# Optimization experiments

Hardware: AMD Instinct MI355X
Metric: run time of the kernel (lower is better)

The kernel has to match this reference:

```python
import jax, jax.numpy as jnp
import numpy as np

EPS = 1e-5

def _bn(h, gamma, beta):
    # training-mode batch norm over dim 0 (biased variance, as torch)
    mu = h.mean(axis=0)
    var = ((h - mu) ** 2).mean(axis=0)
    return (h - mu) * jax.lax.rsqrt(var + EPS) * gamma + beta

def _mlp(h, W1, b1, g1, be1, W2, b2):
    # PyG MLP, num_layers=2: Linear -> BatchNorm -> ReLU -> Linear (dropout=0)
    h = h @ W1 + b1
    h = jax.nn.relu(_bn(h, g1, be1))
    return h @ W2 + b2

def setup_inputs() -> dict:
    key = jax.random.key(0)
    ks = jax.random.split(key, 12)
    N, E = 50000, 800000
    node_dim, edge_dim, hidden = 64, 64, 128
    d_in1 = node_dim + edge_dim   # 128
    d_in2 = node_dim + hidden     # 192
    def lin(k, fi, fo):
        s = 1.0 / np.sqrt(fi)
        return jax.random.uniform(k, (fi, fo), jnp.float32, -s, s)
    inp = {
        "x": jax.random.normal(ks[0], (N, node_dim), jnp.float32),
        "edge_index": jax.random.randint(ks[1], (2, E), 0, N, jnp.int32),
        "edge_attr": jax.random.normal(ks[2], (E, edge_dim), jnp.float32),
        "u": jax.random.normal(ks[3], (1, 16), jnp.float32),
        "batch": jnp.zeros((N,), jnp.int32),
        # node_mlp_1 params
        "W1a": lin(ks[4], d_in1, hidden), "b1a": jnp.zeros((hidden,), jnp.float32),
        "g1a": jnp.ones((hidden,), jnp.float32), "be1a": jnp.zeros((hidden,), jnp.float32),
        "W2a": lin(ks[5], hidden, hidden), "b2a": jnp.zeros((hidden,), jnp.float32),
        # node_mlp_2 params
        "W1b": lin(ks[6], d_in2, hidden), "b1b": jnp.zeros((hidden,), jnp.float32),
        "g1b": jnp.ones((hidden,), jnp.float32), "be1b": jnp.zeros((hidden,), jnp.float32),
        "W2b": lin(ks[7], hidden, node_dim), "b2b": jnp.zeros((node_dim,), jnp.float32),
    }
    return inp

def reference(x, edge_index, edge_attr, u, batch,
              W1a, b1a, g1a, be1a, W2a, b2a,
              W1b, b1b, g1b, be1b, W2b, b2b):
    row, col = edge_index[0], edge_index[1]
    # gather source nodes, concat edge features  -> [E, node_dim+edge_dim]
    out = jnp.concatenate([x[row], edge_attr], axis=1)
    out = _mlp(out, W1a, b1a, g1a, be1a, W2a, b2a)          # [E, hidden]
    out = jax.ops.segment_sum(out, col, num_segments=x.shape[0])  # scatter_add -> [N, hidden]
    out = jnp.concatenate([x, out], axis=1)                  # [N, node_dim+hidden]
    return _mlp(out, W1b, b1b, g1b, be1b, W2b, b2b)          # [N, node_dim]
```

## Files before the change

kernel.cpp:

```cpp
#include <hip/hip_runtime.h>
#include <hip/hip_fp16.h>


typedef _Float16 half8  __attribute__((ext_vector_type(8)));
typedef _Float16 half4h __attribute__((ext_vector_type(4)));
typedef float    floatx4 __attribute__((ext_vector_type(4)));

#define MFMA16(a, b, c) __builtin_amdgcn_mfma_f32_16x16x32_f16(a, b, c, 0, 0, 0)

#define LDS_BARRIER() do { \
    asm volatile("s_waitcnt lgkmcnt(0)" ::: "memory"); \
    __builtin_amdgcn_s_barrier(); \
} while (0)

__device__ __forceinline__ float col_reduce16(float v) {
    v += __shfl_xor(v, 16, 64);
    v += __shfl_xor(v, 32, 64);
    return v;
}

__global__ void k_prep(const float* __restrict__ w1a, const float* __restrict__ w2a,
                       const float* __restrict__ w1b, const float* __restrict__ w2b,
                       _Float16* __restrict__ w1at, _Float16* __restrict__ w2at,
                       _Float16* __restrict__ w1bt, _Float16* __restrict__ w2bt) {
    int i = blockIdx.x * 256 + threadIdx.x;
    if (i < 16384) {
        int n = i >> 7, k = i & 127;
        w1at[n * 128 + k] = (_Float16)w1a[k * 128 + n];
    } else if (i < 32768) {
        int j = i - 16384; int n = j >> 7, k = j & 127;
        w2at[n * 128 + k] = (_Float16)w2a[k * 128 + n];
    } else if (i < 57344) {
        int j = i - 32768; int n = j / 192, k = j - n * 192;
        w1bt[n * 192 + k] = (_Float16)w1b[k * 128 + n];
    } else if (i < 65536) {
        int j = i - 57344; int n = j >> 7, k = j & 127;
        w2bt[n * 128 + k] = (_Float16)w2b[k * 64 + n];
    }
}

__global__ __launch_bounds__(1024) void k_scan(const int* __restrict__ cnt,
                                               int* __restrict__ cur, int N) {
    __shared__ int sp[1024];
    int t = threadIdx.x;
    int chunk = (N + 1023) >> 10;
    int base = t * chunk;
    int s = 0;
    for (int j = 0; j < chunk; j++) {
        int idx = base + j;
        if (idx < N) s += cnt[idx];
    }
    sp[t] = s; __syncthreads();
    for (int off = 1; off < 1024; off <<= 1) {
        int v = (t >= off) ? sp[t - off] : 0;
        __syncthreads();
        sp[t] += v;
        __syncthreads();
    }
    int run = sp[t] - s;
    for (int j = 0; j < chunk; j++) {
        int idx = base + j;
        if (idx < N) { cur[idx] = run; run += cnt[idx]; }
    }
}

__global__ void k_scatter_fin(const int* __restrict__ rowi, const int* __restrict__ coli,
                              int* __restrict__ cur, int2* __restrict__ pairs,
                              const float* __restrict__ sums, const float* __restrict__ sqs,
                              const float* __restrict__ gamma, const float* __restrict__ beta,
                              float* __restrict__ scale, float* __restrict__ shift,
                              float count, int E) {
    int i = blockIdx.x * 512 + threadIdx.x;
    if (i < E) {
        int c = coli[i];
        int p = atomicAdd(&cur[c], 1);
        pairs[p] = make_int2(i, (c << 16) | rowi[i]);
    }
    if (blockIdx.x == 0 && threadIdx.x < 128) {
        int j = threadIdx.x;
        float s = 0.f, ssq = 0.f;
        for (int k = 0; k < 16; k++) { s += sums[k * 128 + j]; ssq += sqs[k * 128 + j]; }
        float mu = s / count;
        float var = ssq / count - mu * mu;
        float sc = gamma[j] * rsqrtf(var + 1e-5f);
        scale[j] = sc;
        shift[j] = beta[j] - mu * sc;
    }
}

__global__ __launch_bounds__(512, 4) void k_edge_stats(
    const float* __restrict__ x, const int* __restrict__ rowi,
    const int* __restrict__ coli,
    const float* __restrict__ ea, const _Float16* __restrict__ w1t,
    float* __restrict__ gsum, float* __restrict__ gsq,
    int* __restrict__ cnt, int nTiles) {
    __shared__ _Float16 sW[128][136];
    __shared__ _Float16 sIn[128][136];
    const int tid = threadIdx.x, lane = tid & 63, wv = tid >> 6;
    const int lm = lane & 15, q = lane >> 4, koff = q * 8;
    const int G = gridDim.x;
    const int e = tid >> 2, part = tid & 3;

    {
        int n = tid >> 2, seg = (tid & 3) * 32;
        const half8* src = (const half8*)(w1t + n * 128 + seg);
        half8* dst = (half8*)&sW[n][seg];
        dst[0] = src[0]; dst[1] = src[1]; dst[2] = src[2]; dst[3] = src[3];
    }
    float sAcc[8], ssAcc[8];
#pragma unroll
    for (int i = 0; i < 8; i++) { sAcc[i] = 0.f; ssAcc[i] = 0.f; }

    int t = blockIdx.x;
    floatx4 pv[8];
    int hc = 0;
    {
        long ge = (long)t * 128 + e;
        const float* src = (part < 2) ? x + (long)rowi[ge] * 64 + part * 32
                                      : ea + ge * 64 + (part - 2) * 32;
#pragma unroll
        for (int i = 0; i < 8; i++) pv[i] = ((const floatx4*)src)[i];
        if (part == 0) hc = coli[ge];
    }
    for (; t < nTiles; t += G) {
        {
            _Float16* dst = &sIn[e][part * 32];
#pragma unroll
            for (int i = 0; i < 8; i++) {
                half4h h = {(_Float16)pv[i][0], (_Float16)pv[i][1],
                            (_Float16)pv[i][2], (_Float16)pv[i][3]};
                *(half4h*)(dst + i * 4) = h;
            }
        }
        LDS_BARRIER();
        if (part == 0) atomicAdd(&cnt[hc], 1);
        int tn = t + G;
        if (tn < nTiles) {
            long ge = (long)tn * 128 + e;
            const float* src = (part < 2) ? x + (long)rowi[ge] * 64 + part * 32
                                          : ea + ge * 64 + (part - 2) * 32;
#pragma unroll
            for (int i = 0; i < 8; i++) pv[i] = ((const floatx4*)src)[i];
            if (part == 0) hc = coli[ge];
        }
        half8 a[4];
#pragma unroll
        for (int kb = 0; kb < 4; kb++)
            a[kb] = *(const half8*)&sIn[wv * 16 + lm][kb * 32 + koff];
#pragma unroll
        for (int nt = 0; nt < 8; nt++) {
            floatx4 acc = {0.f, 0.f, 0.f, 0.f};
            const int c = nt * 16 + lm;
#pragma unroll
            for (int kb = 0; kb < 4; kb++) {
                half8 b = *(const half8*)&sW[c][kb * 32 + koff];
                acc = MFMA16(a[kb], b, acc);
            }
            sAcc[nt]  += acc[0] + acc[1] + acc[2] + acc[3];
            ssAcc[nt] += acc[0]*acc[0] + acc[1]*acc[1] + acc[2]*acc[2] + acc[3]*acc[3];
        }
        LDS_BARRIER();
    }
#pragma unroll
    for (int nt = 0; nt < 8; nt++) {
        float s  = col_reduce16(sAcc[nt]);
        float ss = col_reduce16(ssAcc[nt]);
        if (q == 0) {
            int c = nt * 16 + lm;
            int slot = (blockIdx.x * 8 + wv) & 15;
            unsafeAtomicAdd(&gsum[slot * 128 + c], s);
            unsafeAtomicAdd(&gsq[slot * 128 + c], ss);
        }
    }
}

__global__ void k_finalize(const float* __restrict__ sums, const float* __restrict__ sqs,
                           const float* __restrict__ gamma, const float* __restrict__ beta,
                           float* __restrict__ scale, float* __restrict__ shift, float count) {
    int i = threadIdx.x;
    float s = 0.f, ssq = 0.f;
    for (int j = 0; j < 16; j++) { s += sums[j * 128 + i]; ssq += sqs[j * 128 + i]; }
    float mu = s / count;
    float var = ssq / count - mu * mu;
    float sc = gamma[i] * rsqrtf(var + 1e-5f);
    scale[i] = sc;
    shift[i] = beta[i] - mu * sc;
}

__global__ __launch_bounds__(512, 2) void k_edge_mlp(
    const float* __restrict__ x, const int2* __restrict__ pairs,
    const float* __restrict__ ea, const _Float16* __restrict__ w1t, const _Float16* __restrict__ w2t,
    const float* __restrict__ scale, const float* __restrict__ shift, const float* __restrict__ b2a,
    __half* __restrict__ agg, int nTiles) {
    __shared__ _Float16 sW1[128][136];
    __shared__ _Float16 sW2[128][136];
    __shared__ _Float16 sIn[2][128][136];
    __shared__ float sScale[128], sShift[128], sB2[128];
    __shared__ int sCol[2][128];
    const int tid = threadIdx.x, lane = tid & 63, wv = tid >> 6;
    const int lm = lane & 15, q = lane >> 4, koff = q * 8;
    const int G = gridDim.x;
    const int e = tid >> 2, part = tid & 3;

    {
        int n = tid >> 2, seg = (tid & 3) * 32;
        const half8* s1 = (const half8*)(w1t + n * 128 + seg);
        half8* d1 = (half8*)&sW1[n][seg];
        d1[0] = s1[0]; d1[1] = s1[1]; d1[2] = s1[2]; d1[3] = s1[3];
        const half8* s2 = (const half8*)(w2t + n * 128 + seg);
        half8* d2 = (half8*)&sW2[n][seg];
        d2[0] = s2[0]; d2[1] = s2[1]; d2[2] = s2[2]; d2[3] = s2[3];
    }
    if (tid < 128) { sScale[tid] = scale[tid]; sShift[tid] = shift[tid]; sB2[tid] = b2a[tid]; }

    int t = blockIdx.x;
    {
        long ge = (long)t * 128 + e;
        int2 pr = pairs[ge];
        const float* src = (part < 2) ? x + (long)(pr.y & 0xFFFF) * 64 + part * 32
                                      : ea + (long)pr.x * 64 + (part - 2) * 32;
        _Float16* dst = &sIn[0][e][part * 32];
#pragma unroll
        for (int i = 0; i < 8; i++) {
            floatx4 v = ((const floatx4*)src)[i];
            half4h h = {(_Float16)v[0], (_Float16)v[1], (_Float16)v[2], (_Float16)v[3]};
            *(half4h*)(dst + i * 4) = h;
        }
        if (tid < 128) sCol[0][tid] = (int)(((unsigned)pairs[(long)t * 128 + tid].y) >> 16);
    }
    __syncthreads();
    int p = 0;
    for (; t < nTiles; t += G) {
        half8 a[4];
#pragma unroll
        for (int kb = 0; kb < 4; kb++)
            a[kb] = *(const half8*)&sIn[p][wv * 16 + lm][kb * 32 + koff];
        int myCol[4];
        const int m0 = wv * 16 + q * 4;
#pragma unroll
        for (int r = 0; r < 4; r++) myCol[r] = sCol[p][m0 + r];
        int cp = sCol[p][(q > 0) ? m0 - 1 : m0];
        int cn = sCol[p][(q < 3) ? m0 + 4 : m0 + 3];
        const bool h0 = (q == 0) || (myCol[0] != cp);
        const bool h1 = myCol[1] != myCol[0];
        const bool h2 = myCol[2] != myCol[1];
        const bool h3 = myCol[3] != myCol[2];
        const bool t0 = h1, t1 = h2, t2 = h3;
        const bool t3 = (q == 3) || (myCol[3] != cn);
        const bool c0m = !h0, c1m = c0m && !h1, c2m = c1m && !h2, c3m = c2m && !h3;
        const int F0 = (h0 | h1 | h2 | h3) ? 1 : 0;
        int Fp1 = __shfl(F0, (lane - 16) & 63, 64);
        const bool add1 = (q >= 1) && !F0;
        const int F1 = (F0 || ((q >= 1) && Fp1)) ? 1 : 0;
        const bool add2 = (q >= 2) && !F1;
        const bool useC = (q >= 1) && !h0;

        int tn = t + G; bool hasNext = tn < nTiles;
        floatx4 pv[8]; int pcol = 0;
        if (hasNext) {
            long ge = (long)tn * 128 + e;
            int2 pr = pairs[ge];
            const float* src = (part < 2) ? x + (long)(pr.y & 0xFFFF) * 64 + part * 32
                                          : ea + (long)pr.x * 64 + (part - 2) * 32;
#pragma unroll
            for (int i = 0; i < 8; i++) pv[i] = ((const floatx4*)src)[i];
            if (tid < 128) pcol = (int)(((unsigned)pairs[(long)tn * 128 + tid].y) >> 16);
        }
        floatx4 acc1[8];
#pragma unroll
        for (int nt = 0; nt < 8; nt++) {
            floatx4 acc = {0.f, 0.f, 0.f, 0.f};
            const int c = nt * 16 + lm;
#pragma unroll
            for (int kb = 0; kb < 4; kb++) {
                half8 b = *(const half8*)&sW1[c][kb * 32 + koff];
                acc = MFMA16(a[kb], b, acc);
            }
            acc1[nt] = acc;
        }
        LDS_BARRIER();

        _Float16(*sT)[136] = sIn[p];
#pragma unroll
        for (int nt = 0; nt < 8; nt++) {
            const int c = nt * 16 + lm;
            float sc = sScale[c], sh = sShift[c];
            half4h h;
#pragma unroll
            for (int r = 0; r < 4; r++)
                h[r] = (_Float16)fmaxf(acc1[nt][r] * sc + sh, 0.f);
            *(half4h*)&sT[c][wv * 16 + q * 4] = h;
        }
        half8 a2[4];
#pragma unroll
        for (int kb = 0; kb < 4; kb++) {
#pragma unroll
            for (int j = 0; j < 8; j++)
                a2[kb][j] = sT[kb * 32 + koff + j][wv * 16 + lm];
        }
#pragma unroll
        for (int nt = 0; nt < 8; nt++) {
            floatx4 acc = {0.f, 0.f, 0.f, 0.f};
            const int c = nt * 16 + lm;
#pragma unroll
            for (int kb = 0; kb < 4; kb++) {
                half8 b = *(const half8*)&sW2[c][kb * 32 + koff];
                acc = MFMA16(a2[kb], b, acc);
            }
            acc1[nt] = acc;
        }
        if (hasNext) {
            _Float16* dst = &sIn[p ^ 1][e][part * 32];
#pragma unroll
            for (int i = 0; i < 8; i++) {
                half4h h = {(_Float16)pv[i][0], (_Float16)pv[i][1],
                            (_Float16)pv[i][2], (_Float16)pv[i][3]};
                *(half4h*)(dst + i * 4) = h;
            }
            if (tid < 128) sCol[p ^ 1][tid] = pcol;
        }
#pragma unroll
        for (int nt = 0; nt < 8; nt++) {
            const int c = nt * 16 + lm;
            const int c0 = c & ~1;
            float bb = sB2[c];
            float v0 = acc1[nt][0] + bb, v1 = acc1[nt][1] + bb;
            float v2 = acc1[nt][2] + bb, v3 = acc1[nt][3] + bb;
            float s0 = v0;
            float s1 = h1 ? v1 : (s0 + v1);
            float s2 = h2 ? v2 : (s1 + v2);
            float s3 = h3 ? v3 : (s2 + v3);
            float S = s3;
            float Sp = __shfl(S, (lane - 16) & 63, 64);
            if (add1) S += Sp;
            float Sq = __shfl(S, (lane - 32) & 63, 64);
            if (add2) S += Sq;
            float Cc = __shfl(S, (lane - 16) & 63, 64);
            float C = useC ? Cc : 0.f;
            float f0 = c0m ? (s0 + C) : s0;
            float f1 = c1m ? (s1 + C) : s1;
            float f2 = c2m ? (s2 + C) : s2;
            float f3 = c3m ? (s3 + C) : s3;
            float g0 = __shfl_xor(f0, 1, 64), g1 = __shfl_xor(f1, 1, 64);
            float g2 = __shfl_xor(f2, 1, 64), g3 = __shfl_xor(f3, 1, 64);
            if ((lane & 1) == 0) {
                if (t0) unsafeAtomicAdd((__half2*)&agg[(size_t)myCol[0] * 128 + c0], __floats2half2_rn(f0, g0));
                if (t1) unsafeAtomicAdd((__half2*)&agg[(size_t)myCol[1] * 128 + c0], __floats2half2_rn(f1, g1));
            } else {
                if (t2) unsafeAtomicAdd((__half2*)&agg[(size_t)myCol[2] * 128 + c0], __floats2half2_rn(g2, f2));
                if (t3) unsafeAtomicAdd((__half2*)&agg[(size_t)myCol[3] * 128 + c0], __floats2half2_rn(g3, f3));
            }
        }
        LDS_BARRIER();
        p ^= 1;
    }
}

__global__ __launch_bounds__(512, 2) void k_node_a(
    const float* __restrict__ x, const __half* __restrict__ agg,
    const _Float16* __restrict__ w1bt, float* __restrict__ h3,
    float* __restrict__ gsum, float* __restrict__ gsq, int N) {
    __shared__ _Float16 sIn[128][200];
    __shared__ _Float16 sW[128][200];
    __shared__ float sSum[128], sSq[128];
    const int tid = threadIdx.x, lane = tid & 63, wv = tid >> 6;
    const long e0 = (long)blockIdx.x * 128;

    {
        int n = tid >> 2, seg = (tid & 3) * 48;
        const half8* src = (const half8*)(w1bt + n * 192 + seg);
        half8* dst = (half8*)&sW[n][seg];
        dst[0] = src[0]; dst[1] = src[1]; dst[2] = src[2];
        dst[3] = src[3]; dst[4] = src[4]; dst[5] = src[5];
    }
    if (tid < 128) { sSum[tid] = 0.f; sSq[tid] = 0.f; }
    {
        int m = tid >> 2, seg = tid & 3;
        long gm = e0 + m;
        bool valid = gm < N;
        const float* srcx = x + gm * 64 + seg * 16;
        _Float16* dstx = &sIn[m][seg * 16];
#pragma unroll
        for (int i = 0; i < 4; i++) {
            floatx4 v = {0.f, 0.f, 0.f, 0.f};
            if (valid) v = ((const floatx4*)srcx)[i];
            half4h h = {(_Float16)v[0], (_Float16)v[1], (_Float16)v[2], (_Float16)v[3]};
            *(half4h*)(dstx + i * 4) = h;
        }
        const _Float16* srca = (const _Float16*)agg + gm * 128 + seg * 32;
        _Float16* dsta = &sIn[m][64 + seg * 32];
#pragma unroll
        for (int i = 0; i < 4; i++) {
            half8 v = {0, 0, 0, 0, 0, 0, 0, 0};
            if (valid) v = ((const half8*)srca)[i];
            *(half8*)(dsta + i * 8) = v;
        }
    }
    __syncthreads();

    const int lm = lane & 15, q = lane >> 4, koff = q * 8;
    half8 a[6];
#pragma unroll
    for (int kb = 0; kb < 6; kb++)
        a[kb] = *(const half8*)&sIn[wv * 16 + lm][kb * 32 + koff];
#pragma unroll
    for (int nt = 0; nt < 8; nt++) {
        floatx4 acc = {0.f, 0.f, 0.f, 0.f};
        const int c = nt * 16 + lm;
#pragma unroll
        for (int kb = 0; kb < 6; kb++) {
            half8 b = *(const half8*)&sW[c][kb * 32 + koff];
            acc = MFMA16(a[kb], b, acc);
        }
        float s  = acc[0] + acc[1] + acc[2] + acc[3];
        float ss = acc[0]*acc[0] + acc[1]*acc[1] + acc[2]*acc[2] + acc[3]*acc[3];
        s = col_reduce16(s); ss = col_reduce16(ss);
        if (q == 0) { atomicAdd(&sSum[c], s); atomicAdd(&sSq[c], ss); }
#pragma unroll
        for (int r = 0; r < 4; r++) {
            int m2 = wv * 16 + q * 4 + r;
            long gm2 = e0 + m2;
            if (gm2 < N) h3[gm2 * 128 + c] = acc[r];
        }
    }
    __syncthreads();
    if (tid < 128) {
        int slot = blockIdx.x & 15;
        unsafeAtomicAdd(&gsum[slot * 128 + tid], sSum[tid]);
        unsafeAtomicAdd(&gsq[slot * 128 + tid], sSq[tid]);
    }
}

__global__ __launch_bounds__(512, 2) void k_node_b(
    const float* __restrict__ h3, const _Float16* __restrict__ w2bt,
    const float* __restrict__ scale, const float* __restrict__ shift,
    const float* __restrict__ b2b, float* __restrict__ out, int N) {
    __shared__ _Float16 sH[128][136];
    __shared__ _Float16 sW[64][136];
    const int tid = threadIdx.x, lane = tid & 63, wv = tid >> 6;
    const long e0 = (long)blockIdx.x * 128;

    {
        int n = tid >> 3, seg = (tid & 7) * 16;
        const half8* src = (const half8*)(w2bt + n * 128 + seg);
        half8* dst = (half8*)&sW[n][seg];
        dst[0] = src[0]; dst[1] = src[1];
    }
    {
        int m = tid >> 2, seg = (tid & 3) * 32;
        long gm = e0 + m;
        bool valid = gm < N;
        const float* src = h3 + gm * 128 + seg;
        _Float16* dst = &sH[m][seg];
#pragma unroll
        for (int i = 0; i < 8; i++) {
            floatx4 v = {0.f, 0.f, 0.f, 0.f};
            if (valid) v = ((const floatx4*)src)[i];
            floatx4 sc = ((const floatx4*)(scale + seg))[i];
            floatx4 sh = ((const floatx4*)(shift + seg))[i];
            half4h h;
#pragma unroll
            for (int j = 0; j < 4; j++)
                h[j] = (_Float16)fmaxf(v[j] * sc[j] + sh[j], 0.f);
            *(half4h*)(dst + i * 4) = h;
        }
    }
    __syncthreads();

    const int lm = lane & 15, q = lane >> 4, koff = q * 8;
    half8 a[4];
#pragma unroll
    for (int kb = 0; kb < 4; kb++)
        a[kb] = *(const half8*)&sH[wv * 16 + lm][kb * 32 + koff];
#pragma unroll
    for (int nt = 0; nt < 4; nt++) {
        floatx4 acc = {0.f, 0.f, 0.f, 0.f};
        const int c = nt * 16 + lm;
#pragma unroll
        for (int kb = 0; kb < 4; kb++) {
            half8 b = *(const half8*)&sW[c][kb * 32 + koff];
            acc = MFMA16(a[kb], b, acc);
        }
        float bb = b2b[c];
#pragma unroll
        for (int r = 0; r < 4; r++) {
            int m2 = wv * 16 + q * 4 + r;
            long gm2 = e0 + m2;
            if (gm2 < N) out[gm2 * 64 + c] = acc[r] + bb;
        }
    }
}

extern "C" void kernel_launch(void* const* d_in, const int* in_sizes, int n_in,
                              void* d_out, int out_size, void* d_ws, size_t ws_size,
                              hipStream_t stream) {
    const float* x    = (const float*)d_in[0];
    const int*   eidx = (const int*)d_in[1];
    const float* ea   = (const float*)d_in[2];
    const float* W1a  = (const float*)d_in[5];
    const float* g1a  = (const float*)d_in[7];
    const float* be1a = (const float*)d_in[8];
    const float* W2a  = (const float*)d_in[9];
    const float* b2a  = (const float*)d_in[10];
    const float* W1b  = (const float*)d_in[11];
    const float* g1b  = (const float*)d_in[13];
    const float* be1b = (const float*)d_in[14];
    const float* W2b  = (const float*)d_in[15];
    const float* b2b  = (const float*)d_in[16];
    const int N = in_sizes[0] / 64;
    const int E = in_sizes[2] / 64;
    const int* rowi = eidx;
    const int* coli = eidx + E;

    float* ws   = (float*)d_ws;
    __half* agg = (__half*)ws;
    float* h3   = ws + (size_t)N * 64;
    float* st   = h3 + (size_t)N * 128;
    float* sumE = st,        * sqE = st + 2048;
    float* sumN = st + 4096, * sqN = st + 6144;
    float* scE  = st + 8192, * shE = st + 8320;
    float* scN  = st + 8448, * shN = st + 8576;
    _Float16* wh   = (_Float16*)(st + 8704);
    _Float16* w1at = wh;
    _Float16* w2at = wh + 16384;
    _Float16* w1bt = wh + 32768;
    _Float16* w2bt = wh + 57344;
    int* cnt  = (int*)(wh + 65536);
    int* cur  = cnt + N;
    int2* pairs = (int2*)(cur + N);

    hipMemsetAsync(agg, 0, (size_t)N * 128 * sizeof(__half), stream);
    hipMemsetAsync(st, 0, 8192 * sizeof(float), stream);
    hipMemsetAsync(cnt, 0, (size_t)N * sizeof(int), stream);
    k_prep<<<256, 256, 0, stream>>>(W1a, W2a, W1b, W2b, w1at, w2at, w1bt, w2bt);

    int nTilesE = E / 128;
    int nbl = (N + 127) / 128;
    int nbE = (E + 511) / 512;
    k_edge_stats<<<512, 512, 0, stream>>>(x, rowi, coli, ea, w1at, sumE, sqE, cnt, nTilesE);
    k_scan<<<1, 1024, 0, stream>>>(cnt, cur, N);
    k_scatter_fin<<<nbE, 512, 0, stream>>>(rowi, coli, cur, pairs, sumE, sqE, g1a, be1a,
                                           scE, shE, (float)E, E);
    k_edge_mlp<<<256, 512, 0, stream>>>(x, pairs, ea, w1at, w2at, scE, shE, b2a, agg, nTilesE);
    k_node_a<<<nbl, 512, 0, stream>>>(x, agg, w1bt, h3, sumN, sqN, N);
    k_finalize<<<1, 128, 0, stream>>>(sumN, sqN, g1b, be1b, scN, shN, (float)N);
    k_node_b<<<nbl, 512, 0, stream>>>(h3, w2bt, scN, shN, b2b, (float*)d_out, N);
}
```

Measured before the change: 733.0 us.

## Make edge-kernel LDS tiles wave-private and drop block-wide barriers

In both edge kernels, each wave now writes and reads only its own 16 rows of the shared input tile, so the per-tile block barriers become simple lgkmcnt waits. The edge MLP kernel also drops its double buffer and the transposed intermediate. It writes the BN+ReLU activations row-major into the same wave-private rows using pairwise shuffles, and reads them back as vectors instead of strided scalars. Scale, shift and bias are held in registers, and neighbour column indices come from lane shuffles instead of shared memory. This removes 512-thread barrier stalls and some LDS traffic, at the cost of more registers and less overlap between loading the next tile and the current MFMA work.

```diff
diff --git a/kernel.cpp b/kernel.cpp
--- a/kernel.cpp
+++ b/kernel.cpp
@@ -4,14 +4,12 @@
 
 typedef _Float16 half8  __attribute__((ext_vector_type(8)));
 typedef _Float16 half4h __attribute__((ext_vector_type(4)));
+typedef _Float16 half2h __attribute__((ext_vector_type(2)));
 typedef float    floatx4 __attribute__((ext_vector_type(4)));
 
 #define MFMA16(a, b, c) __builtin_amdgcn_mfma_f32_16x16x32_f16(a, b, c, 0, 0, 0)
 
-#define LDS_BARRIER() do { \
-    asm volatile("s_waitcnt lgkmcnt(0)" ::: "memory"); \
-    __builtin_amdgcn_s_barrier(); \
-} while (0)
+#define LGKM0() asm volatile("s_waitcnt lgkmcnt(0)" ::: "memory")
 
 __device__ __forceinline__ float col_reduce16(float v) {
     v += __shfl_xor(v, 16, 64);
@@ -100,6 +98,7 @@
     const int lm = lane & 15, q = lane >> 4, koff = q * 8;
     const int G = gridDim.x;
     const int e = tid >> 2, part = tid & 3;
+    const int row = wv * 16 + lm;
 
     {
         int n = tid >> 2, seg = (tid & 3) * 32;
@@ -107,6 +106,8 @@
         half8* dst = (half8*)&sW[n][seg];
         dst[0] = src[0]; dst[1] = src[1]; dst[2] = src[2]; dst[3] = src[3];
     }
+    __syncthreads();
+
     float sAcc[8], ssAcc[8];
 #pragma unroll
     for (int i = 0; i < 8; i++) { sAcc[i] = 0.f; ssAcc[i] = 0.f; }
@@ -132,7 +133,6 @@
                 *(half4h*)(dst + i * 4) = h;
             }
         }
-        LDS_BARRIER();
         if (part == 0) atomicAdd(&cnt[hc], 1);
         int tn = t + G;
         if (tn < nTiles) {
@@ -143,10 +143,11 @@
             for (int i = 0; i < 8; i++) pv[i] = ((const floatx4*)src)[i];
             if (part == 0) hc = coli[ge];
         }
+        LGKM0();
         half8 a[4];
 #pragma unroll
         for (int kb = 0; kb < 4; kb++)
-            a[kb] = *(const half8*)&sIn[wv * 16 + lm][kb * 32 + koff];
+            a[kb] = *(const half8*)&sIn[row][kb * 32 + koff];
 #pragma unroll
         for (int nt = 0; nt < 8; nt++) {
             floatx4 acc = {0.f, 0.f, 0.f, 0.f};
@@ -159,7 +160,6 @@
             sAcc[nt]  += acc[0] + acc[1] + acc[2] + acc[3];
             ssAcc[nt] += acc[0]*acc[0] + acc[1]*acc[1] + acc[2]*acc[2] + acc[3]*acc[3];
         }
-        LDS_BARRIER();
     }
 #pragma unroll
     for (int nt = 0; nt < 8; nt++) {
@@ -194,13 +194,13 @@
     __half* __restrict__ agg, int nTiles) {
     __shared__ _Float16 sW1[128][136];
     __shared__ _Float16 sW2[128][136];
-    __shared__ _Float16 sIn[2][128][136];
-    __shared__ float sScale[128], sShift[128], sB2[128];
-    __shared__ int sCol[2][128];
+    __shared__ _Float16 sIn[128][136];
     const int tid = threadIdx.x, lane = tid & 63, wv = tid >> 6;
     const int lm = lane & 15, q = lane >> 4, koff = q * 8;
     const int G = gridDim.x;
     const int e = tid >> 2, part = tid & 3;
+    const int row = wv * 16 + lm;
+    const int m0 = wv * 16 + q * 4;
 
     {
         int n = tid >> 2, seg = (tid & 3) * 32;
@@ -211,36 +211,41 @@
         half8* d2 = (half8*)&sW2[n][seg];
         d2[0] = s2[0]; d2[1] = s2[1]; d2[2] = s2[2]; d2[3] = s2[3];
     }
-    if (tid < 128) { sScale[tid] = scale[tid]; sShift[tid] = shift[tid]; sB2[tid] = b2a[tid]; }
+    float scl[8], shf[8], b2[8];
+#pragma unroll
+    for (int nt = 0; nt < 8; nt++) {
+        scl[nt] = scale[nt * 16 + lm];
+        shf[nt] = shift[nt * 16 + lm];
+        b2[nt]  = b2a[nt * 16 + lm];
+    }
+    __syncthreads();
 
     int t = blockIdx.x;
+    floatx4 pv[8]; int mc[4];
     {
         long ge = (long)t * 128 + e;
         int2 pr = pairs[ge];
         const float* src = (part < 2) ? x + (long)(pr.y & 0xFFFF) * 64 + part * 32
                                       : ea + (long)pr.x * 64 + (part - 2) * 32;
-        _Float16* dst = &sIn[0][e][part * 32];
-#pragma unroll
-        for (int i = 0; i < 8; i++) {
-            floatx4 v = ((const floatx4*)src)[i];
-            half4h h = {(_Float16)v[0], (_Float16)v[1], (_Float16)v[2], (_Float16)v[3]};
-            *(half4h*)(dst + i * 4) = h;
-        }
-        if (tid < 128) sCol[0][tid] = (int)(((unsigned)pairs[(long)t * 128 + tid].y) >> 16);
-    }
-    __syncthreads();
-    int p = 0;
+#pragma unroll
+        for (int i = 0; i < 8; i++) pv[i] = ((const floatx4*)src)[i];
+#pragma unroll
+        for (int r = 0; r < 4; r++)
+            mc[r] = (int)(((unsigned)pairs[(long)t * 128 + m0 + r].y) >> 16);
+    }
     for (; t < nTiles; t += G) {
-        half8 a[4];
-#pragma unroll
-        for (int kb = 0; kb < 4; kb++)
-            a[kb] = *(const half8*)&sIn[p][wv * 16 + lm][kb * 32 + koff];
-        int myCol[4];
-        const int m0 = wv * 16 + q * 4;
-#pragma unroll
-        for (int r = 0; r < 4; r++) myCol[r] = sCol[p][m0 + r];
-        int cp = sCol[p][(q > 0) ? m0 - 1 : m0];
-        int cn = sCol[p][(q < 3) ? m0 + 4 : m0 + 3];
+        {
+            _Float16* dst = &sIn[e][part * 32];
+#pragma unroll
+            for (int i = 0; i < 8; i++) {
+                half4h h = {(_Float16)pv[i][0], (_Float16)pv[i][1],
+                            (_Float16)pv[i][2], (_Float16)pv[i][3]};
+                *(half4h*)(dst + i * 4) = h;
+            }
+        }
+        int myCol[4] = {mc[0], mc[1], mc[2], mc[3]};
+        int cp = __shfl(myCol[3], (lane - 16) & 63, 64);
+        int cn = __shfl(myCol[0], (lane + 16) & 63, 64);
         const bool h0 = (q == 0) || (myCol[0] != cp);
         const bool h1 = myCol[1] != myCol[0];
         const bool h2 = myCol[2] != myCol[1];
@@ -256,7 +261,6 @@
         const bool useC = (q >= 1) && !h0;
 
         int tn = t + G; bool hasNext = tn < nTiles;
-        floatx4 pv[8]; int pcol = 0;
         if (hasNext) {
             long ge = (long)tn * 128 + e;
             int2 pr = pairs[ge];
@@ -264,8 +268,15 @@
                                           : ea + (long)pr.x * 64 + (part - 2) * 32;
 #pragma unroll
             for (int i = 0; i < 8; i++) pv[i] = ((const floatx4*)src)[i];
-            if (tid < 128) pcol = (int)(((unsigned)pairs[(long)tn * 128 + tid].y) >> 16);
-        }
+#pragma unroll
+            for (int r = 0; r < 4; r++)
+                mc[r] = (int)(((unsigned)pairs[(long)tn * 128 + m0 + r].y) >> 16);
+        }
+        LGKM0();
+        half8 a[4];
+#pragma unroll
+        for (int kb = 0; kb < 4; kb++)
+            a[kb] = *(const half8*)&sIn[row][kb * 32 + koff];
         floatx4 acc1[8];
 #pragma unroll
         for (int nt = 0; nt < 8; nt++) {
@@ -278,26 +289,23 @@
             }
             acc1[nt] = acc;
         }
-        LDS_BARRIER();
-
-        _Float16(*sT)[136] = sIn[p];
 #pragma unroll
         for (int nt = 0; nt < 8; nt++) {
-            const int c = nt * 16 + lm;
-            float sc = sScale[c], sh = sShift[c];
-            half4h h;
-#pragma unroll
-            for (int r = 0; r < 4; r++)
-                h[r] = (_Float16)fmaxf(acc1[nt][r] * sc + sh, 0.f);
-            *(half4h*)&sT[c][wv * 16 + q * 4] = h;
-        }
+#pragma unroll
+            for (int r = 0; r < 4; r++) {
+                float h = fmaxf(acc1[nt][r] * scl[nt] + shf[nt], 0.f);
+                float g = __shfl_xor(h, 1, 64);
+                if (!(lane & 1)) {
+                    half2h pr2 = {(_Float16)h, (_Float16)g};
+                    *(half2h*)&sIn[m0 + r][nt * 16 + lm] = pr2;
+                }
+            }
+        }
+        LGKM0();
         half8 a2[4];
 #pragma unroll
-        for (int kb = 0; kb < 4; kb++) {
-#pragma unroll
-            for (int j = 0; j < 8; j++)
-                a2[kb][j] = sT[kb * 32 + koff + j][wv * 16 + lm];
-        }
+        for (int kb = 0; kb < 4; kb++)
+            a2[kb] = *(const half8*)&sIn[row][kb * 32 + koff];
 #pragma unroll
         for (int nt = 0; nt < 8; nt++) {
             floatx4 acc = {0.f, 0.f, 0.f, 0.f};
@@ -309,21 +317,11 @@
             }
             acc1[nt] = acc;
         }
-        if (hasNext) {
-            _Float16* dst = &sIn[p ^ 1][e][part * 32];
-#pragma unroll
-            for (int i = 0; i < 8; i++) {
-                half4h h = {(_Float16)pv[i][0], (_Float16)pv[i][1],
-                            (_Float16)pv[i][2], (_Float16)pv[i][3]};
-                *(half4h*)(dst + i * 4) = h;
-            }
-            if (tid < 128) sCol[p ^ 1][tid] = pcol;
-        }
 #pragma unroll
         for (int nt = 0; nt < 8; nt++) {
             const int c = nt * 16 + lm;
             const int c0 = c & ~1;
-            float bb = sB2[c];
+            float bb = b2[nt];
             float v0 = acc1[nt][0] + bb, v1 = acc1[nt][1] + bb;
             float v2 = acc1[nt][2] + bb, v3 = acc1[nt][3] + bb;
             float s0 = v0;
@@ -351,8 +349,6 @@
                 if (t3) unsafeAtomicAdd((__half2*)&agg[(size_t)myCol[3] * 128 + c0], __floats2half2_rn(g3, f3));
             }
         }
-        LDS_BARRIER();
-        p ^= 1;
     }
 }
 
```

Result: faster. 713.9 us (-2.6%).
